# Kernel tuning notes

Measured on AMD Instinct MI355X. Metric: run time of the kernel, lower is better.

Reference implementation:

```python
import jax, jax.numpy as jnp
import numpy as np

N2 = 524288   # raw batch (2B)
F = 256       # raw feature dim; concat of halves -> D = 2F
D = 512       # input_dim (gated feature dim)
H_GATE = 64
H_EXP = 128


def _init(key, shape, fan_in):
    return jax.random.normal(key, shape, jnp.float32) / np.sqrt(fan_in)


def setup_inputs() -> dict:
    key = jax.random.key(0)
    ks = jax.random.split(key, 13)
    x = jax.random.normal(ks[0], (N2, F), jnp.float32)
    # gate: Linear(D,64) -> ReLU -> Linear(64,2)
    gw1 = _init(ks[1], (D, H_GATE), D)
    gb1 = jnp.zeros((H_GATE,), jnp.float32)
    gw2 = _init(ks[2], (H_GATE, 2), H_GATE)
    gb2 = jnp.zeros((2,), jnp.float32)
    # expert_a: Linear(D,128) -> ReLU -> Linear(128,2)
    aw1 = _init(ks[3], (D, H_EXP), D)
    ab1 = jnp.zeros((H_EXP,), jnp.float32)
    aw2 = _init(ks[4], (H_EXP, 2), H_EXP)
    ab2 = jnp.zeros((2,), jnp.float32)
    # expert_b: same shapes
    bw1 = _init(ks[5], (D, H_EXP), D)
    bb1 = jnp.zeros((H_EXP,), jnp.float32)
    bw2 = _init(ks[6], (H_EXP, 2), H_EXP)
    bb2 = jnp.zeros((2,), jnp.float32)
    return dict(x=x, gw1=gw1, gb1=gb1, gw2=gw2, gb2=gb2,
                aw1=aw1, ab1=ab1, aw2=aw2, ab2=ab2,
                bw1=bw1, bb1=bb1, bw2=bw2, bb2=bb2)


def reference(x, gw1, gb1, gw2, gb2, aw1, ab1, aw2, ab2, bw1, bb1, bw2, bb2):
    # backbone = identity; concat first and second batch halves along features
    n = x.shape[0]
    xf = jnp.concatenate([x[: n // 2], x[n // 2 :]], axis=1)  # [B, D]
    # hard gate: argmax over 2 logits
    gate_logits = jax.nn.relu(xf @ gw1 + gb1) @ gw2 + gb2  # [B, 2]
    gate_idx = jnp.argmax(gate_logits, axis=1)  # [B]
    # run both tiny experts densely, then mask (same math as masked dispatch)
    out_a = jax.nn.relu(xf @ aw1 + ab1) @ aw2 + ab2  # [B, 2]
    out_b = jax.nn.relu(xf @ bw1 + bb1) @ bw2 + bb2  # [B, 2]
    m_a = (gate_idx == 0)[:, None]
    # rows routed to expert_a fill cols 0:2, rows routed to expert_b fill cols 2:4
    return jnp.concatenate(
        [jnp.where(m_a, out_a, 0.0), jnp.where(m_a, 0.0, out_b)], axis=1
    )  # [B, 4]
```

## Files before the change

### kernel.cpp

```cpp
#include <hip/hip_runtime.h>
#include <hip/hip_bf16.h>

#define HALF_ROWS 262144
#define TAU 0.04f
#define BT_OFF 1024
#define LIST_OFF (BT_OFF + 320 * 512 * 2)

typedef __attribute__((ext_vector_type(8))) short s16x8;
typedef __attribute__((ext_vector_type(4))) float f32x4;

__device__ __forceinline__ unsigned short f2bf(float f) {
  union { float f; unsigned u; } v; v.f = f;
  unsigned r = v.u + 0x7fffu + ((v.u >> 16) & 1u);
  return (unsigned short)(r >> 16);
}

#define GLOAD_LDS16(g, p) \
  __builtin_amdgcn_global_load_lds((const __attribute__((address_space(1))) void*)(g), \
                                   (__attribute__((address_space(3))) void*)(p), 16, 0, 0)

__device__ __forceinline__ s16x8 cvt8(const f32x4& a, const f32x4& b) {
  union { int i[4]; s16x8 v; } u;
  asm("v_cvt_pk_bf16_f32 %0, %1, %2" : "=v"(u.i[0]) : "v"(a[0]), "v"(a[1]));
  asm("v_cvt_pk_bf16_f32 %0, %1, %2" : "=v"(u.i[1]) : "v"(a[2]), "v"(a[3]));
  asm("v_cvt_pk_bf16_f32 %0, %1, %2" : "=v"(u.i[2]) : "v"(b[0]), "v"(b[1]));
  asm("v_cvt_pk_bf16_f32 %0, %1, %2" : "=v"(u.i[3]) : "v"(b[2]), "v"(b[3]));
  return u.v;
}

__global__ void moe_prep(const float* __restrict__ gw1, const float* __restrict__ aw1,
                         const float* __restrict__ bw1, unsigned short* __restrict__ Bf,
                         unsigned* __restrict__ cnt) {
  if (blockIdx.x == 0 && threadIdx.x == 0) *cnt = 0u;
  int idx = blockIdx.x * 512 + threadIdx.x;
  int j = idx & 7, l = (idx >> 3) & 63, ks = (idx >> 9) & 15, cb = idx >> 13;
  int col = cb * 16 + (l & 15);
  int k = ks * 32 + ((l >> 4) << 3) + j;
  float v;
  if (col < 64)       v = gw1[k * 64 + col];
  else if (col < 192) v = aw1[k * 128 + (col - 64)];
  else                v = bw1[k * 128 + (col - 192)];
  Bf[idx] = f2bf(v);
}

__global__ __launch_bounds__(1024, 4) void moe_main(
    const float* __restrict__ x, const unsigned short* __restrict__ Bf,
    const float* __restrict__ gb1, const float* __restrict__ gw2, const float* __restrict__ gb2,
    const float* __restrict__ ab1, const float* __restrict__ aw2, const float* __restrict__ ab2,
    const float* __restrict__ bb1, const float* __restrict__ bw2, const float* __restrict__ bb2,
    float* __restrict__ out, unsigned* __restrict__ cnt, unsigned* __restrict__ list, int cap) {
  __shared__ char Bl[3][20480];

  const int tid = threadIdx.x;
  const int w = tid >> 6, l = tid & 63;
  const int lo = l & 15, hi = l >> 4;
  const long row0 = (long)blockIdx.x * 256 + w * 16 + lo;
  const float* ap = x + row0 * 256 + hi * 8;

  const unsigned short* bsrc = Bf + l * 8;
  auto issueB = [&](int kc) {
    char* dst = Bl[kc % 3];
    GLOAD_LDS16(bsrc + ((size_t)(w * 16 + kc) << 9), dst + w * 1024);
    if (w < 4)
      GLOAD_LDS16(bsrc + ((size_t)((16 + w) * 16 + kc) << 9), dst + (16 + w) * 1024);
  };

  f32x4 cur0, cur1, nxt0, nxt1;
  auto loadA = [&](int kc, f32x4& d0, f32x4& d1) {
    const float* p = ap + (kc & 7) * 32 + (kc >= 8 ? (long)HALF_ROWS * 256 : 0L);
    d0 = *(const f32x4*)p;
    d1 = *(const f32x4*)(p + 4);
  };

  f32x4 acc[20];
#pragma unroll
  for (int ct = 0; ct < 20; ++ct) acc[ct] = (f32x4){0.f, 0.f, 0.f, 0.f};

  loadA(0, cur0, cur1);
  issueB(0);
  issueB(1);
  if (w < 4) asm volatile("s_waitcnt vmcnt(2)" ::: "memory");
  else       asm volatile("s_waitcnt vmcnt(1)" ::: "memory");
  __builtin_amdgcn_s_barrier();

#pragma unroll 1
  for (int kc = 0; kc < 16; ++kc) {
    if (kc + 2 < 16) issueB(kc + 2);
    if (kc + 1 < 16) loadA(kc + 1, nxt0, nxt1);
    asm volatile("" ::: "memory");
    s16x8 af = cvt8(cur0, cur1);
    const char* buf = Bl[kc % 3];
#pragma unroll
    for (int ct = 0; ct < 20; ++ct) {
      s16x8 bf = *(const s16x8*)(buf + (ct << 10) + (l << 4));
      acc[ct] = __builtin_amdgcn_mfma_f32_16x16x32_bf16(af, bf, acc[ct], 0, 0, 0);
    }
    cur0 = nxt0; cur1 = nxt1;
    if (kc < 15) __builtin_amdgcn_s_barrier();
  }

  float pg0[4] = {0,0,0,0}, pg1[4] = {0,0,0,0};
  float pa0[4] = {0,0,0,0}, pa1[4] = {0,0,0,0};
  float pq0[4] = {0,0,0,0}, pq1[4] = {0,0,0,0};
#pragma unroll
  for (int ct = 0; ct < 20; ++ct) {
    int col = ct * 16 + lo;
    float b1, w0, w1;
    if (ct < 4)       { b1 = gb1[col];        w0 = gw2[col * 2];        w1 = gw2[col * 2 + 1]; }
    else if (ct < 12) { int c = col - 64;  b1 = ab1[c]; w0 = aw2[c * 2]; w1 = aw2[c * 2 + 1]; }
    else              { int c = col - 192; b1 = bb1[c]; w0 = bw2[c * 2]; w1 = bw2[c * 2 + 1]; }
#pragma unroll
    for (int j = 0; j < 4; ++j) {
      float h = fmaxf(acc[ct][j] + b1, 0.f);
      float t0 = h * w0, t1 = h * w1;
      if (ct < 4)       { pg0[j] += t0; pg1[j] += t1; }
      else if (ct < 12) { pa0[j] += t0; pa1[j] += t1; }
      else              { pq0[j] += t0; pq1[j] += t1; }
    }
  }
#pragma unroll
  for (int m = 1; m < 16; m <<= 1)
#pragma unroll
    for (int j = 0; j < 4; ++j) {
      pg0[j] += __shfl_xor(pg0[j], m); pg1[j] += __shfl_xor(pg1[j], m);
      pa0[j] += __shfl_xor(pa0[j], m); pa1[j] += __shfl_xor(pa1[j], m);
      pq0[j] += __shfl_xor(pq0[j], m); pq1[j] += __shfl_xor(pq1[j], m);
    }
  if (lo == 0) {
    float g2a = gb2[0], g2b = gb2[1];
    float a2a = ab2[0], a2b = ab2[1];
    float b2a = bb2[0], b2b = bb2[1];
#pragma unroll
    for (int j = 0; j < 4; ++j) {
      long grow = ((long)blockIdx.x * 256 + w * 16) + hi * 4 + j;
      float gl0 = pg0[j] + g2a, gl1 = pg1[j] + g2b;
      float fa0 = pa0[j] + a2a, fa1 = pa1[j] + a2b;
      float fb0 = pq0[j] + b2a, fb1 = pq1[j] + b2b;
      bool m0 = gl0 >= gl1;
      f32x4 o;
      o[0] = m0 ? fa0 : 0.f; o[1] = m0 ? fa1 : 0.f;
      o[2] = m0 ? 0.f : fb0; o[3] = m0 ? 0.f : fb1;
      *(f32x4*)(out + grow * 4) = o;
      float diff = gl0 - gl1;
      if (fabsf(diff) < TAU && cap > 0) {
        unsigned u = atomicAdd(cnt, 1u);
        if (u < (unsigned)cap) {
          unsigned* e = list + (size_t)u * 8;
          e[0] = (unsigned)grow;
          float* ef = (float*)(e + 4);
          ef[0] = fa0; ef[1] = fa1; ef[2] = fb0; ef[3] = fb1;
        }
      }
    }
  }
}

__global__ void moe_fixup(const float* __restrict__ x,
                          const float* __restrict__ gw1, const float* __restrict__ gb1,
                          const float* __restrict__ gw2, const float* __restrict__ gb2,
                          float* __restrict__ out, const unsigned* __restrict__ cnt,
                          const unsigned* __restrict__ list, int cap) {
  unsigned n = *cnt;
  if (n > (unsigned)cap) n = (unsigned)cap;
  const int l = threadIdx.x & 63;
  const int wid = blockIdx.x * (blockDim.x >> 6) + (threadIdx.x >> 6);
  const int nw = gridDim.x * (blockDim.x >> 6);
  for (unsigned e = wid; e < n; e += nw) {
    const unsigned* ent = list + (size_t)e * 8;
    unsigned row = ent[0];
    const float* ef = (const float*)(ent + 4);
    const float* xr0 = x + (long)row * 256;
    const float* xr1 = x + ((long)row + HALF_ROWS) * 256;
    double a[8] = {0, 0, 0, 0, 0, 0, 0, 0};
#pragma unroll 2
    for (int d = 0; d < 256; d += 8)
#pragma unroll
      for (int q = 0; q < 8; ++q)
        a[q] += (double)xr0[d + q] * (double)gw1[(d + q) * 64 + l];
#pragma unroll 2
    for (int d = 0; d < 256; d += 8)
#pragma unroll
      for (int q = 0; q < 8; ++q)
        a[q] += (double)xr1[d + q] * (double)gw1[(d + 256 + q) * 64 + l];
    double h = ((a[0] + a[1]) + (a[2] + a[3])) + ((a[4] + a[5]) + (a[6] + a[7]))
             + (double)gb1[l];
    h = h > 0.0 ? h : 0.0;
    double t0 = h * (double)gw2[l * 2];
    double t1 = h * (double)gw2[l * 2 + 1];
#pragma unroll
    for (int m = 1; m < 64; m <<= 1) {
      t0 += __shfl_xor(t0, m);
      t1 += __shfl_xor(t1, m);
    }
    if (l == 0) {
      bool m0 = (t0 + (double)gb2[0]) >= (t1 + (double)gb2[1]);
      f32x4 o;
      o[0] = m0 ? ef[0] : 0.f; o[1] = m0 ? ef[1] : 0.f;
      o[2] = m0 ? 0.f : ef[2]; o[3] = m0 ? 0.f : ef[3];
      *(f32x4*)(out + (size_t)row * 4) = o;
    }
  }
}

extern "C" void kernel_launch(void* const* d_in, const int* in_sizes, int n_in,
                              void* d_out, int out_size, void* d_ws, size_t ws_size,
                              hipStream_t stream) {
  const float* x   = (const float*)d_in[0];
  const float* gw1 = (const float*)d_in[1];
  const float* gb1 = (const float*)d_in[2];
  const float* gw2 = (const float*)d_in[3];
  const float* gb2 = (const float*)d_in[4];
  const float* aw1 = (const float*)d_in[5];
  const float* ab1 = (const float*)d_in[6];
  const float* aw2 = (const float*)d_in[7];
  const float* ab2 = (const float*)d_in[8];
  const float* bw1 = (const float*)d_in[9];
  const float* bb1 = (const float*)d_in[10];
  const float* bw2 = (const float*)d_in[11];
  const float* bb2 = (const float*)d_in[12];
  float* out = (float*)d_out;

  unsigned char* ws = (unsigned char*)d_ws;
  unsigned* cnt = (unsigned*)ws;
  unsigned short* Bf = (unsigned short*)(ws + BT_OFF);
  unsigned* list = (unsigned*)(ws + LIST_OFF);
  long cap_l = ((long)ws_size - (long)LIST_OFF) / 32;
  int cap = cap_l < 0 ? 0 : (cap_l > 262144 ? 262144 : (int)cap_l);

  moe_prep<<<320, 512, 0, stream>>>(gw1, aw1, bw1, Bf, cnt);
  moe_main<<<1024, 1024, 0, stream>>>(x, Bf, gb1, gw2, gb2, ab1, aw2, ab2,
                                      bb1, bw2, bb2, out, cnt, list, cap);
  moe_fixup<<<2048, 256, 0, stream>>>(x, gw1, gb1, gw2, gb2, out, cnt, list, cap);
}
```

Measured before the change: 329.5 us.

## Read bf16 weight fragments directly from global memory instead of LDS staging

Removes the triple-buffered LDS staging of the bf16 weight matrix, along with its async global-to-LDS loads and per-step barriers. Each wave now loads its B fragments straight from global memory and relies on L1/L2 caching of the small 320KB weight buffer. Blocks shrink to 512 threads covering 128 rows, and the grid doubles to 2048. This drops synchronisation and LDS traffic, but every wave now issues its own 20 global loads per k-step, which risks memory latency stalls and higher cache pressure.

```diff
diff --git a/kernel.cpp b/kernel.cpp
--- a/kernel.cpp
+++ b/kernel.cpp
@@ -14,10 +14,6 @@
   unsigned r = v.u + 0x7fffu + ((v.u >> 16) & 1u);
   return (unsigned short)(r >> 16);
 }
-
-#define GLOAD_LDS16(g, p) \
-  __builtin_amdgcn_global_load_lds((const __attribute__((address_space(1))) void*)(g), \
-                                   (__attribute__((address_space(3))) void*)(p), 16, 0, 0)
 
 __device__ __forceinline__ s16x8 cvt8(const f32x4& a, const f32x4& b) {
   union { int i[4]; s16x8 v; } u;
@@ -43,60 +39,43 @@
   Bf[idx] = f2bf(v);
 }
 
-__global__ __launch_bounds__(1024, 4) void moe_main(
+__global__ __launch_bounds__(512, 2) void moe_main(
     const float* __restrict__ x, const unsigned short* __restrict__ Bf,
     const float* __restrict__ gb1, const float* __restrict__ gw2, const float* __restrict__ gb2,
     const float* __restrict__ ab1, const float* __restrict__ aw2, const float* __restrict__ ab2,
     const float* __restrict__ bb1, const float* __restrict__ bw2, const float* __restrict__ bb2,
     float* __restrict__ out, unsigned* __restrict__ cnt, unsigned* __restrict__ list, int cap) {
-  __shared__ char Bl[3][20480];
-
   const int tid = threadIdx.x;
   const int w = tid >> 6, l = tid & 63;
   const int lo = l & 15, hi = l >> 4;
-  const long row0 = (long)blockIdx.x * 256 + w * 16 + lo;
-  const float* ap = x + row0 * 256 + hi * 8;
-
-  const unsigned short* bsrc = Bf + l * 8;
-  auto issueB = [&](int kc) {
-    char* dst = Bl[kc % 3];
-    GLOAD_LDS16(bsrc + ((size_t)(w * 16 + kc) << 9), dst + w * 1024);
-    if (w < 4)
-      GLOAD_LDS16(bsrc + ((size_t)((16 + w) * 16 + kc) << 9), dst + (16 + w) * 1024);
-  };
-
-  f32x4 cur0, cur1, nxt0, nxt1;
-  auto loadA = [&](int kc, f32x4& d0, f32x4& d1) {
-    const float* p = ap + (kc & 7) * 32 + (kc >= 8 ? (long)HALF_ROWS * 256 : 0L);
-    d0 = *(const f32x4*)p;
-    d1 = *(const f32x4*)(p + 4);
-  };
+  const long r0 = (long)blockIdx.x * 128 + w * 16;
+  const float* ap0 = x + (r0 + lo) * 256 + hi * 8;
+  const float* ap1 = ap0 + (long)HALF_ROWS * 256;
+  const unsigned short* bp = Bf + l * 8;
 
   f32x4 acc[20];
 #pragma unroll
   for (int ct = 0; ct < 20; ++ct) acc[ct] = (f32x4){0.f, 0.f, 0.f, 0.f};
 
-  loadA(0, cur0, cur1);
-  issueB(0);
-  issueB(1);
-  if (w < 4) asm volatile("s_waitcnt vmcnt(2)" ::: "memory");
-  else       asm volatile("s_waitcnt vmcnt(1)" ::: "memory");
-  __builtin_amdgcn_s_barrier();
+  f32x4 a0 = *(const f32x4*)ap0;
+  f32x4 a1 = *(const f32x4*)(ap0 + 4);
 
 #pragma unroll 1
   for (int kc = 0; kc < 16; ++kc) {
-    if (kc + 2 < 16) issueB(kc + 2);
-    if (kc + 1 < 16) loadA(kc + 1, nxt0, nxt1);
-    asm volatile("" ::: "memory");
-    s16x8 af = cvt8(cur0, cur1);
-    const char* buf = Bl[kc % 3];
+    f32x4 n0, n1;
+    if (kc < 15) {
+      const float* np = (kc < 7) ? ap0 + (kc + 1) * 32 : ap1 + (kc - 7) * 32;
+      n0 = *(const f32x4*)np;
+      n1 = *(const f32x4*)(np + 4);
+    }
+    s16x8 af = cvt8(a0, a1);
+    const unsigned short* bq = bp + ((size_t)kc << 9);
 #pragma unroll
     for (int ct = 0; ct < 20; ++ct) {
-      s16x8 bf = *(const s16x8*)(buf + (ct << 10) + (l << 4));
+      s16x8 bf = *(const s16x8*)(bq + ((size_t)ct << 13));
       acc[ct] = __builtin_amdgcn_mfma_f32_16x16x32_bf16(af, bf, acc[ct], 0, 0, 0);
     }
-    cur0 = nxt0; cur1 = nxt1;
-    if (kc < 15) __builtin_amdgcn_s_barrier();
+    a0 = n0; a1 = n1;
   }
 
   float pg0[4] = {0,0,0,0}, pg1[4] = {0,0,0,0};
@@ -127,15 +106,12 @@
       pq0[j] += __shfl_xor(pq0[j], m); pq1[j] += __shfl_xor(pq1[j], m);
     }
   if (lo == 0) {
-    float g2a = gb2[0], g2b = gb2[1];
-    float a2a = ab2[0], a2b = ab2[1];
-    float b2a = bb2[0], b2b = bb2[1];
 #pragma unroll
     for (int j = 0; j < 4; ++j) {
-      long grow = ((long)blockIdx.x * 256 + w * 16) + hi * 4 + j;
-      float gl0 = pg0[j] + g2a, gl1 = pg1[j] + g2b;
-      float fa0 = pa0[j] + a2a, fa1 = pa1[j] + a2b;
-      float fb0 = pq0[j] + b2a, fb1 = pq1[j] + b2b;
+      long grow = r0 + hi * 4 + j;
+      float gl0 = pg0[j] + gb2[0], gl1 = pg1[j] + gb2[1];
+      float fa0 = pa0[j] + ab2[0], fa1 = pa1[j] + ab2[1];
+      float fb0 = pq0[j] + bb2[0], fb1 = pq1[j] + bb2[1];
       bool m0 = gl0 >= gl1;
       f32x4 o;
       o[0] = m0 ? fa0 : 0.f; o[1] = m0 ? fa1 : 0.f;
@@ -228,7 +204,7 @@
   int cap = cap_l < 0 ? 0 : (cap_l > 262144 ? 262144 : (int)cap_l);
 
   moe_prep<<<320, 512, 0, stream>>>(gw1, aw1, bw1, Bf, cnt);
-  moe_main<<<1024, 1024, 0, stream>>>(x, Bf, gb1, gw2, gb2, ab1, aw2, ab2,
-                                      bb1, bw2, bb2, out, cnt, list, cap);
+  moe_main<<<2048, 512, 0, stream>>>(x, Bf, gb1, gw2, gb2, ab1, aw2, ab2,
+                                     bb1, bw2, bb2, out, cnt, list, cap);
   moe_fixup<<<2048, 256, 0, stream>>>(x, gw1, gb1, gw2, gb2, out, cnt, list, cap);
 }
```

Result: slower. 420.8 us (+27.7%).
